# Kernel optimization log

Hardware: AMD Instinct MI355X
Metric: run time of the kernel (lower is better)

Reference implementation:

```python
import jax, jax.numpy as jnp
import numpy as np

K = 4096          # in_features
N = 11008         # out_features
GROUP = 128       # scale group size along K
PACK = 16
BATCH, SEQ = 2, 4096


def setup_inputs() -> dict:
    key = jax.random.key(0)
    k1, k2, k3, k4 = jax.random.split(key, 4)
    x = jax.random.normal(k1, (BATCH, SEQ, K), dtype=jnp.float16)
    # valid ternary codes in {0,1,2} encoding w = code - 1 in {-1,0,+1}
    codes = jax.random.randint(k2, (K, N), 0, 3, dtype=jnp.int32)
    codes = codes.reshape(K // PACK, PACK, N)
    shifts = (2 * jnp.arange(PACK, dtype=jnp.int32))[None, :, None]
    packed_weight = jnp.sum(codes << shifts, axis=1).astype(jnp.int32)  # (K//16, N)
    scales = (jax.random.uniform(k3, (K // GROUP, N), dtype=jnp.float32) * 0.1 + 0.01).astype(jnp.float16)
    bias = (jax.random.normal(k4, (N,), dtype=jnp.float32) * 0.01).astype(jnp.float16)
    return {"x": x, "packed_weight": packed_weight, "scales": scales, "bias": bias}


def _dequant(packed_weight, scales):
    # unpack 16 two-bit codes per int32 along K
    shifts = (2 * jnp.arange(PACK, dtype=jnp.int32))[None, :, None]
    codes = (packed_weight[:, None, :] >> shifts) & 3        # (K//16, 16, N)
    Kp = packed_weight.shape[0] * PACK
    Nn = packed_weight.shape[1]
    w = (codes.astype(jnp.float16) - jnp.float16(1.0)).reshape(Kp, Nn)  # ternary {-1,0,1}
    scale_full = jnp.repeat(scales, GROUP, axis=0)            # (K, N) group-wise gamma
    return w * scale_full


def reference(x, packed_weight, scales, bias):
    Kp = packed_weight.shape[0] * PACK
    Nn = packed_weight.shape[1]
    w = _dequant(packed_weight, scales)                       # (K, N) fp16
    x2 = x.reshape(-1, Kp).astype(jnp.float16)                # (M, K)
    out = jnp.dot(x2, w, preferred_element_type=jnp.float32).astype(jnp.float16)
    out = out + bias
    return out.reshape(*x.shape[:-1], Nn)
```

## Files before the change

### kernel.cpp

```cpp
#include <hip/hip_runtime.h>
#include <stdint.h>

#define K_DIM 4096
#define N_DIM 11008
#define M_DIM 8192
#define BM 128
#define BN 128
#define BK 32
#define ASTRIDE 32
#define BSTRIDE 40
#define NSLAB (K_DIM / BK)

typedef _Float16 half8  __attribute__((ext_vector_type(8)));
typedef _Float16 half2v __attribute__((ext_vector_type(2)));
typedef float    floatx4 __attribute__((ext_vector_type(4)));

__global__ __launch_bounds__(256, 2) void ternary_gemm(
    const float* __restrict__ x,
    const int*   __restrict__ pw,
    const float* __restrict__ scales,
    const float* __restrict__ bias,
    float*       __restrict__ out)
{
    __shared__ __align__(16) _Float16 lds_a[BM * ASTRIDE];
    __shared__ __align__(16) _Float16 lds_b[BN * BSTRIDE];

    const int tid  = threadIdx.x;
    const int lane = tid & 63;
    const int wave = tid >> 6;

    const int n0 = blockIdx.x * BN;
    const int m0 = blockIdx.y * BM;

    const int wm = (wave & 1) * 64;
    const int wn = (wave >> 1) * 64;

    const int nb  = tid & 127;
    const int kpi = tid >> 7;
    const int*   pwp = pw + (size_t)kpi * N_DIM + n0 + nb;
    const float* scp = scales + n0 + nb;
    _Float16* bl = lds_b + nb * BSTRIDE + kpi * 16;

    floatx4 acc[4][4];
    #pragma unroll
    for (int i = 0; i < 4; ++i)
        #pragma unroll
        for (int j = 0; j < 4; ++j)
            acc[i][j] = floatx4{0.f, 0.f, 0.f, 0.f};

    const int lr = lane & 15;
    const int qk = (lane >> 4) * 8;

    for (int slab = 0; slab < NSLAB; ++slab) {
        const int k0 = slab * BK;

        #pragma unroll
        for (int i = 0; i < 4; ++i) {
            const int idx = tid + i * 256;
            const int row = idx >> 3;
            const int kq  = (idx & 7) * 4;
            float4 v4 = *(const float4*)(x + (size_t)(m0 + row) * K_DIM + k0 + kq);
            half2v h0; h0[0] = (_Float16)v4.x; h0[1] = (_Float16)v4.y;
            half2v h1; h1[0] = (_Float16)v4.z; h1[1] = (_Float16)v4.w;
            *(uint2*)(lds_a + row * ASTRIDE + kq) =
                make_uint2(__builtin_bit_cast(uint32_t, h0),
                           __builtin_bit_cast(uint32_t, h1));
        }

        uint32_t v  = (uint32_t)pwp[(size_t)slab * 2 * N_DIM];
        _Float16 sh = (_Float16)scp[(size_t)(slab >> 2) * N_DIM];
        uint32_t sbits = (uint32_t)__builtin_bit_cast(unsigned short, sh);
        uint32_t tmpl = sbits | (((sbits >> 8) ^ 0x80u) << 24);

        uint32_t q[8];
        #pragma unroll
        for (int j = 0; j < 8; ++j) {
            uint32_t t4 = (v >> (4 * j)) & 0xFu;
            uint32_t sp = (t4 | (t4 << 14)) & 0x00030003u;
            uint32_t sel = ((sp & 0x00010001u) << 1) | ((0x00030003u - sp) << 8);
            q[j] = __builtin_amdgcn_perm(tmpl, tmpl, sel);
        }
        *(uint4*)(bl)     = make_uint4(q[0], q[1], q[2], q[3]);
        *(uint4*)(bl + 8) = make_uint4(q[4], q[5], q[6], q[7]);

        __syncthreads();

        half8 af[4], bfr[4];
        #pragma unroll
        for (int t = 0; t < 4; ++t) {
            af[t]  = *(const half8*)&lds_a[(wm + t * 16 + lr) * ASTRIDE + qk];
            bfr[t] = *(const half8*)&lds_b[(wn + t * 16 + lr) * BSTRIDE + qk];
        }
        #pragma unroll
        for (int mt = 0; mt < 4; ++mt)
            #pragma unroll
            for (int nt = 0; nt < 4; ++nt)
                acc[mt][nt] = __builtin_amdgcn_mfma_f32_16x16x32_f16(
                    af[mt], bfr[nt], acc[mt][nt], 0, 0, 0);

        __syncthreads();
    }

    float bv[4];
    #pragma unroll
    for (int nt = 0; nt < 4; ++nt) bv[nt] = bias[n0 + wn + nt * 16 + lr];

    const int rbase = (lane >> 4) * 4;
    #pragma unroll
    for (int mt = 0; mt < 4; ++mt) {
        #pragma unroll
        for (int nt = 0; nt < 4; ++nt) {
            const int col = n0 + wn + nt * 16 + lr;
            float* op = out + (size_t)(m0 + wm + mt * 16 + rbase) * N_DIM + col;
            floatx4 a = acc[mt][nt];
            #pragma unroll
            for (int r = 0; r < 4; ++r)
                op[(size_t)r * N_DIM] = a[r] + bv[nt];
        }
    }
}

extern "C" void kernel_launch(void* const* d_in, const int* in_sizes, int n_in,
                              void* d_out, int out_size, void* d_ws, size_t ws_size,
                              hipStream_t stream) {
    const float* x  = (const float*)d_in[0];
    const int*   pw = (const int*)d_in[1];
    const float* sc = (const float*)d_in[2];
    const float* bs = (const float*)d_in[3];
    float* out = (float*)d_out;

    dim3 grid(N_DIM / BN, M_DIM / BM);
    ternary_gemm<<<grid, 256, 0, stream>>>(x, pw, sc, bs, out);
}
```

Measured before the change: 1.263 ms.

## Pre-convert activations and dequantize weights into workspace, then async-load GEMM

When enough workspace is available, the launch now runs a kernel that converts x to fp16 once and a kernel that dequantizes the ternary weights into a K-contiguous fp16 matrix. A simpler GEMM then streams both operands straight into LDS with global_load_lds 16-byte copies. This removes the repeated fp32 A loads and the per-tile weight unpacking that every block used to redo. In exchange it adds two extra kernel launches, roughly 150 MB of extra workspace traffic, and an LDS layout without padding that may cause bank conflicts. The original fused kernel stays as the fallback when workspace is too small.

```diff
diff --git a/kernel.cpp b/kernel.cpp
--- a/kernel.cpp
+++ b/kernel.cpp
@@ -7,13 +7,147 @@
 #define BM 128
 #define BN 128
 #define BK 32
+#define NSLAB (K_DIM / BK)
+
 #define ASTRIDE 32
 #define BSTRIDE 40
-#define NSLAB (K_DIM / BK)
 
 typedef _Float16 half8  __attribute__((ext_vector_type(8)));
 typedef _Float16 half2v __attribute__((ext_vector_type(2)));
 typedef float    floatx4 __attribute__((ext_vector_type(4)));
+
+#define WS_A_BYTES ((size_t)M_DIM * K_DIM * 2)
+#define WS_B_BYTES ((size_t)N_DIM * K_DIM * 2)
+#define WS_NEEDED  (WS_A_BYTES + WS_B_BYTES)
+
+__device__ __forceinline__ void async_lds16(const void* g, void* l) {
+    __builtin_amdgcn_global_load_lds(
+        (const __attribute__((address_space(1))) uint32_t*)g,
+        (__attribute__((address_space(3))) uint32_t*)l, 16, 0, 0);
+}
+
+__global__ __launch_bounds__(256) void cvt_a(const float* __restrict__ x,
+                                             _Float16* __restrict__ xh) {
+    const size_t i = ((size_t)blockIdx.x * 256 + threadIdx.x) * 8;
+    const float4 a = *(const float4*)(x + i);
+    const float4 b = *(const float4*)(x + i + 4);
+    half8 h;
+    h[0] = (_Float16)a.x; h[1] = (_Float16)a.y; h[2] = (_Float16)a.z; h[3] = (_Float16)a.w;
+    h[4] = (_Float16)b.x; h[5] = (_Float16)b.y; h[6] = (_Float16)b.z; h[7] = (_Float16)b.w;
+    *(half8*)(xh + i) = h;
+}
+
+__global__ __launch_bounds__(256) void dequant_b(const int* __restrict__ pw,
+                                                 const float* __restrict__ scales,
+                                                 _Float16* __restrict__ wh) {
+    const int n   = blockIdx.x * 64 + (threadIdx.x & 63);
+    const int kpo = threadIdx.x >> 6;
+    const int kpb = blockIdx.y * 64;
+    #pragma unroll 4
+    for (int i = 0; i < 16; ++i) {
+        const int kp = kpb + i * 4 + kpo;
+        const uint32_t v = (uint32_t)pw[(size_t)kp * N_DIM + n];
+        const _Float16 sh = (_Float16)scales[(size_t)(kp >> 3) * N_DIM + n];
+        const uint32_t sbits = (uint32_t)__builtin_bit_cast(unsigned short, sh);
+        const uint32_t tmpl = sbits | (((sbits >> 8) ^ 0x80u) << 24);
+        uint32_t q[8];
+        #pragma unroll
+        for (int j = 0; j < 8; ++j) {
+            uint32_t t4 = (v >> (4 * j)) & 0xFu;
+            uint32_t sp = (t4 | (t4 << 14)) & 0x00030003u;
+            uint32_t sel = ((sp & 0x00010001u) << 1) | ((0x00030003u - sp) << 8);
+            q[j] = __builtin_amdgcn_perm(tmpl, tmpl, sel);
+        }
+        _Float16* dst = wh + (size_t)n * K_DIM + kp * 16;
+        *(uint4*)(dst)     = make_uint4(q[0], q[1], q[2], q[3]);
+        *(uint4*)(dst + 8) = make_uint4(q[4], q[5], q[6], q[7]);
+    }
+}
+
+__global__ __launch_bounds__(256, 2) void ternary_gemm_ws(
+    const _Float16* __restrict__ xh,
+    const _Float16* __restrict__ wh,
+    const float*    __restrict__ bias,
+    float*          __restrict__ out)
+{
+    __shared__ __align__(16) _Float16 lds_a[BM * BK];
+    __shared__ __align__(16) _Float16 lds_b[BN * BK];
+
+    const int tid  = threadIdx.x;
+    const int lane = tid & 63;
+    const int wave = tid >> 6;
+
+    const int n0 = blockIdx.x * BN;
+    const int m0 = blockIdx.y * BM;
+    const int wm = (wave & 1) * 64;
+    const int wn = (wave >> 1) * 64;
+
+    const int srow = tid >> 2;
+    const int skq  = (tid & 3) * 8;
+
+    const _Float16* ga0 = xh + (size_t)(m0 + srow) * K_DIM + skq;
+    const _Float16* ga1 = ga0 + (size_t)64 * K_DIM;
+    const _Float16* gb0 = wh + (size_t)(n0 + srow) * K_DIM + skq;
+    const _Float16* gb1 = gb0 + (size_t)64 * K_DIM;
+    _Float16* la0 = lds_a + tid * 8;
+    _Float16* la1 = lds_a + 2048 + tid * 8;
+    _Float16* lb0 = lds_b + tid * 8;
+    _Float16* lb1 = lds_b + 2048 + tid * 8;
+
+    floatx4 acc[4][4];
+    #pragma unroll
+    for (int i = 0; i < 4; ++i)
+        #pragma unroll
+        for (int j = 0; j < 4; ++j)
+            acc[i][j] = floatx4{0.f, 0.f, 0.f, 0.f};
+
+    const int lr = lane & 15;
+    const int qk = (lane >> 4) * 8;
+
+    for (int slab = 0; slab < NSLAB; ++slab) {
+        const int k0 = slab * BK;
+
+        async_lds16(ga0 + k0, la0);
+        async_lds16(ga1 + k0, la1);
+        async_lds16(gb0 + k0, lb0);
+        async_lds16(gb1 + k0, lb1);
+
+        __syncthreads();
+
+        half8 af[4], bfr[4];
+        #pragma unroll
+        for (int t = 0; t < 4; ++t) {
+            af[t]  = *(const half8*)&lds_a[(wm + t * 16 + lr) * BK + qk];
+            bfr[t] = *(const half8*)&lds_b[(wn + t * 16 + lr) * BK + qk];
+        }
+        #pragma unroll
+        for (int mt = 0; mt < 4; ++mt)
+            #pragma unroll
+            for (int nt = 0; nt < 4; ++nt)
+                acc[mt][nt] = __builtin_amdgcn_mfma_f32_16x16x32_f16(
+                    af[mt], bfr[nt], acc[mt][nt], 0, 0, 0);
+
+        __syncthreads();
+    }
+
+    float bv[4];
+    #pragma unroll
+    for (int nt = 0; nt < 4; ++nt) bv[nt] = bias[n0 + wn + nt * 16 + lr];
+
+    const int rbase = (lane >> 4) * 4;
+    #pragma unroll
+    for (int mt = 0; mt < 4; ++mt) {
+        #pragma unroll
+        for (int nt = 0; nt < 4; ++nt) {
+            const int col = n0 + wn + nt * 16 + lr;
+            float* op = out + (size_t)(m0 + wm + mt * 16 + rbase) * N_DIM + col;
+            floatx4 a = acc[mt][nt];
+            #pragma unroll
+            for (int r = 0; r < 4; ++r)
+                op[(size_t)r * N_DIM] = a[r] + bv[nt];
+        }
+    }
+}
 
 __global__ __launch_bounds__(256, 2) void ternary_gemm(
     const float* __restrict__ x,
@@ -129,6 +263,13 @@
     const float* bs = (const float*)d_in[3];
     float* out = (float*)d_out;
 
-    dim3 grid(N_DIM / BN, M_DIM / BM);
-    ternary_gemm<<<grid, 256, 0, stream>>>(x, pw, sc, bs, out);
-}
+    if (d_ws != nullptr && ws_size >= WS_NEEDED) {
+        _Float16* xh = (_Float16*)d_ws;
+        _Float16* wh = (_Float16*)((char*)d_ws + WS_A_BYTES);
+        cvt_a<<<dim3((unsigned)((size_t)M_DIM * K_DIM / (256 * 8))), 256, 0, stream>>>(x, xh);
+        dequant_b<<<dim3(N_DIM / 64, 4), 256, 0, stream>>>(pw, sc, wh);
+        ternary_gemm_ws<<<dim3(N_DIM / BN, M_DIM / BM), 256, 0, stream>>>(xh, wh, bs, out);
+    } else {
+        ternary_gemm<<<dim3(N_DIM / BN, M_DIM / BM), 256, 0, stream>>>(x, pw, sc, bs, out);
+    }
+}
```

New measurement: 1.690 ms. +33.8%, slower.
